# Optimization experiments

Hardware: AMD Instinct MI355X
Metric: run time of the kernel (lower is better)

## Reference

```python
import jax, jax.numpy as jnp
import numpy as np

N = 24000      # total nodes (8000 per node type)
IN_DIM = 128
OUT_DIM = 128
H = 8          # heads
DK = 16        # out_dim // n_heads
T = 3          # node types (hard-coded in edge_attention)
R = 34         # relations (etypes 0..33 per the etype->ntype rules)
EPR = 10000    # edges per relation (DGL applies edge fn per etype)


def _rel_node_types(num_rel):
    # src/dst node type per relation, transcribed from edge_attention
    src_nt = np.array([0 if r <= 9 else (1 if r <= 21 else 2) for r in range(num_rel)], np.int32)
    def _dnt(r):
        if r <= 2 or 10 <= r <= 13 or 22 <= r <= 24:
            return 0
        if 3 <= r <= 6 or 14 <= r <= 17 or 25 <= r <= 28:
            return 1
        return 2
    dst_nt = np.array([_dnt(r) for r in range(num_rel)], np.int32)
    return src_nt, dst_nt

SRC_NT, DST_NT = _rel_node_types(R)


def setup_inputs() -> dict:
    rng = np.random.default_rng(0)
    Nt = N // T  # nodes of type t live in [t*Nt, (t+1)*Nt)
    src = np.stack([rng.integers(SRC_NT[r] * Nt, (SRC_NT[r] + 1) * Nt, EPR) for r in range(R)]).astype(np.int32)
    dst = np.stack([rng.integers(DST_NT[r] * Nt, (DST_NT[r] + 1) * Nt, EPR) for r in range(R)]).astype(np.int32)
    ks = jax.random.split(jax.random.key(0), 10)
    lin = 1.0 / np.sqrt(IN_DIM)
    return {
        'x': jax.random.normal(ks[0], (N, IN_DIM), jnp.float32),
        'src': jnp.asarray(src),
        'dst': jnp.asarray(dst),
        'Wk': jax.random.normal(ks[1], (T, IN_DIM, OUT_DIM), jnp.float32) * lin,
        'bk': jnp.zeros((T, OUT_DIM), jnp.float32),
        'Wq': jax.random.normal(ks[2], (T, IN_DIM, OUT_DIM), jnp.float32) * lin,
        'bq': jnp.zeros((T, OUT_DIM), jnp.float32),
        'Wv': jax.random.normal(ks[3], (T, IN_DIM, OUT_DIM), jnp.float32) * lin,
        'bv': jnp.zeros((T, OUT_DIM), jnp.float32),
        'Wa': jax.random.normal(ks[4], (T, OUT_DIM, OUT_DIM), jnp.float32) * lin,
        'ba': jnp.zeros((T, OUT_DIM), jnp.float32),
        'rel_att': jax.random.normal(ks[5], (R, H, DK, DK), jnp.float32) / np.sqrt(DK),
        'rel_msg': jax.random.normal(ks[6], (R, H, DK, DK), jnp.float32) / np.sqrt(DK),
        'rel_pri': jnp.ones((R, H), jnp.float32),
        'nta': jnp.ones((T,), jnp.float32),
        'nta1': jnp.ones((T,), jnp.float32),
        'skip': jnp.ones((T,), jnp.float32),
        'weight': jnp.ones((1,), jnp.float32),
        'attn_w': jax.random.normal(ks[7], (2 * DK,), jnp.float32) * 0.1,
    }


def reference(x, src, dst, Wk, bk, Wq, bq, Wv, bv, Wa, ba, rel_att, rel_msg, rel_pri, nta, nta1, skip, weight, attn_w):
    ntype = jnp.repeat(jnp.arange(T), N // T)  # node type per node id
    ridx = jnp.arange(N)

    def typed_lin(h, W, b):
        # per-node-type Linear: compute all T projections, select by node type
        return (jnp.einsum('ni,tio->tno', h, W) + b[:, None, :])[ntype, ridx]

    k = typed_lin(x, Wk, bk).reshape(N, H, DK)
    q = typed_lin(x, Wq, bq).reshape(N, H, DK)
    v = typed_lin(x, Wv, bv).reshape(N, H, DK)

    k_src = k[src]                                   # [R, Epr, H, DK]
    q_dst = q[dst]                                   # [R, Epr, H, DK]
    key_t = jnp.einsum('rehd,rhdf->rehf', k_src, rel_att)
    a = (q_dst * key_t).sum(-1) * rel_pri[:, None, :] / np.sqrt(DK)   # [R, Epr, H]
    val = jnp.einsum('rehd,rhdf->rehf', v[src], rel_msg)              # [R, Epr, H, DK]

    # GAT-style concat attention: attn_fc(cat(att_dst*q, att_src*k)) split into two dots
    wq, wk = attn_w[:DK], attn_w[DK:]
    na = jax.nn.leaky_relu(nta1[DST_NT][:, None, None] * (q_dst @ wq)
                           + nta[SRC_NT][:, None, None] * (k_src @ wk))  # [R, Epr, H]

    beta = jax.nn.sigmoid(weight[0])
    s = (a + beta * na).reshape(R * EPR, H)

    # per-(relation, dst-node) segment softmax (DGL mailbox softmax per etype)
    seg = (jnp.arange(R)[:, None] * N + dst).reshape(-1)
    m = jax.ops.segment_max(s, seg, num_segments=R * N)
    e = jnp.exp(s - m[seg])
    den = jax.ops.segment_sum(e, seg, num_segments=R * N)
    att = e / den[seg]

    vf = val.reshape(R * EPR, H, DK)
    h = jax.ops.segment_sum(att[:, :, None] * vf, seg, num_segments=R * N).reshape(R, N, OUT_DIM)

    # cross_reducer='mean': average over relations that delivered messages to a node
    cnt = jax.ops.segment_sum(jnp.ones((R * EPR,), x.dtype), seg, num_segments=R * N).reshape(R, N)
    nrel = jnp.maximum((cnt > 0).astype(x.dtype).sum(0), 1.0)
    t = h.sum(0) / nrel[:, None]                      # [N, OUT_DIM]

    trans = (jnp.einsum('no,top->tnp', t, Wa) + ba[:, None, :])[ntype, ridx]
    alpha = jax.nn.sigmoid(skip)[ntype][:, None]
    return trans * alpha + x * (1.0 - alpha)
```

## Files before the change

kernel.cpp:

```cpp
#include <hip/hip_runtime.h>

#define NN   24000
#define NTP  8000
#define HH   8
#define DKK  16
#define RR   34
#define EPRN 10000
#define NE   (RR*EPRN)
#define NB   (RR*NTP)
#define CAP  16
#define NSCAT ((NE+255)/256)

typedef short short8 __attribute__((ext_vector_type(8)));
typedef float f32x4  __attribute__((ext_vector_type(4)));
typedef _Float16 h2v __attribute__((ext_vector_type(2)));

#if defined(__has_builtin)
# if __has_builtin(__builtin_amdgcn_fdot2)
#  define USE_FDOT2 1
# endif
#endif
#ifndef USE_FDOT2
# define USE_FDOT2 0
#endif

__device__ __forceinline__ int src_nt(int r){ return r<=9?0:(r<=21?1:2); }
__device__ __forceinline__ int dst_nt(int r){
    if (r<=2)  return 0;
    if (r<=6)  return 1;
    if (r<=9)  return 2;
    if (r<=13) return 0;
    if (r<=17) return 1;
    if (r<=21) return 2;
    if (r<=24) return 0;
    if (r<=28) return 1;
    return 2;
}

__device__ __forceinline__ unsigned short bf16rne(float a){
    unsigned int u = __float_as_uint(a);
    u += 0x7fffu + ((u >> 16) & 1u);
    return (unsigned short)(u >> 16);
}
__device__ __forceinline__ unsigned int bf2pack(float a, float b){
    unsigned int ua = __float_as_uint(a);
    unsigned int ub = __float_as_uint(b);
    ua += 0x7fffu + ((ua >> 16) & 1u);
    ub += 0x7fffu + ((ub >> 16) & 1u);
    return (ua >> 16) | (ub & 0xffff0000u);
}
__device__ __forceinline__ unsigned short f16bits(float a){
    _Float16 h = (_Float16)a;
    return __builtin_bit_cast(unsigned short, h);
}

__global__ __launch_bounds__(256) void prep_kernel(
    const float* __restrict__ Wk, const float* __restrict__ Wq,
    const float* __restrict__ Wv, const float* __restrict__ Wa,
    int* __restrict__ counts, unsigned short* __restrict__ wfrag)
{
    const int gid = blockIdx.x * 256 + threadIdx.x;
    if (gid < NB) counts[gid] = 0;
    if (blockIdx.x < 96) {
        const int tile = blockIdx.x * 4 + (threadIdx.x >> 6);
        const int lane = threadIdx.x & 63;
        const float* W;
        int s, n;
        if (tile < 288) {
            s = tile & 3;
            n = (tile >> 2) & 7;
            const int mat = (tile >> 5) % 3;
            const int tau = tile / 96;
            W = (mat == 0 ? Wk : (mat == 1 ? Wq : Wv)) + (size_t)tau * 16384;
        } else {
            const int t2 = tile - 288;
            s = t2 & 3;
            n = (t2 >> 2) & 7;
            const int tau = t2 >> 5;
            W = Wa + (size_t)tau * 16384;
        }
        const int k0  = s * 32 + (lane >> 4) * 8;
        const int col = n * 16 + (lane & 15);
        unsigned short* dstp = wfrag + (size_t)tile * 512 + lane * 8;
        #pragma unroll
        for (int i = 0; i < 8; i++)
            dstp[i] = bf16rne(W[(size_t)(k0 + i) * 128 + col]);
    }
}

__global__ __launch_bounds__(256) void work1(
    const float* __restrict__ x,
    const float* __restrict__ bk, const float* __restrict__ bq,
    const float* __restrict__ bv,
    const unsigned short* __restrict__ wfrag,
    const int* __restrict__ src, const int* __restrict__ dst,
    int* __restrict__ counts, int* __restrict__ esrc16,
    float* __restrict__ qo, unsigned short* __restrict__ kvh)
{
    __shared__ float qs[4][16][132];
    __shared__ unsigned short ksh[4][16][264];

    if (blockIdx.x >= 375) {
        int e = (blockIdx.x - 375) * 256 + threadIdx.x;
        if (e < NE) {
            int r = e / EPRN;
            int b = r * NTP + (dst[e] - dst_nt(r) * NTP);
            int pos = atomicAdd(&counts[b], 1);
            if (pos < CAP) esrc16[(size_t)b * CAP + pos] = src[e];
        }
        return;
    }

    const int rb   = blockIdx.x * 64;
    const int tau  = rb / NTP;
    const int w    = threadIdx.x >> 6;
    const int lane = threadIdx.x & 63;
    const int m    = lane & 15;
    const int quad = lane >> 4;

    short8 af[4];
    {
        const float* xrow = x + (size_t)(rb + w * 16 + m) * 128;
        #pragma unroll
        for (int s = 0; s < 4; s++) {
            float4 f0 = *(const float4*)(xrow + s * 32 + quad * 8);
            float4 f1 = *(const float4*)(xrow + s * 32 + quad * 8 + 4);
            union { unsigned int u[4]; short8 v; } pk;
            pk.u[0] = bf2pack(f0.x, f0.y); pk.u[1] = bf2pack(f0.z, f0.w);
            pk.u[2] = bf2pack(f1.x, f1.y); pk.u[3] = bf2pack(f1.z, f1.w);
            af[s] = pk.v;
        }
    }

    #pragma unroll
    for (int mat = 0; mat < 3; mat++) {
        const float* bias = (mat == 0 ? bk : (mat == 1 ? bq : bv)) + tau * 128;
        #pragma unroll
        for (int n = 0; n < 8; n++) {
            float bb = bias[n * 16 + m];
            f32x4 acc = {bb, bb, bb, bb};
            #pragma unroll
            for (int s = 0; s < 4; s++) {
                const int tile = ((tau * 3 + mat) * 8 + n) * 4 + s;
                short8 bf = *(const short8*)(wfrag + (size_t)tile * 512 + lane * 8);
                acc = __builtin_amdgcn_mfma_f32_16x16x32_bf16(af[s], bf, acc, 0, 0, 0);
            }
            if (mat == 1) {
                #pragma unroll
                for (int i = 0; i < 4; i++) qs[w][quad * 4 + i][n * 16 + m] = acc[i];
            } else {
                const int off = n * 32 + (mat == 0 ? 0 : 16) + m;
                #pragma unroll
                for (int i = 0; i < 4; i++) ksh[w][quad * 4 + i][off] = f16bits(acc[i]);
            }
        }
        if (mat == 1) {
            __syncthreads();
            #pragma unroll
            for (int j = 0; j < 8; j++) {
                const int id = lane + 64 * j;
                const int row = id >> 5, c4 = id & 31;
                float4 v = *(const float4*)(&qs[w][row][c4 * 4]);
                *(float4*)(qo + (size_t)(rb + w * 16 + row) * 128 + c4 * 4) = v;
            }
        }
    }
    __syncthreads();
    #pragma unroll
    for (int j = 0; j < 8; j++) {
        const int id = lane + 64 * j;
        const int row = id >> 5, c8 = id & 31;
        uint4 u = *(const uint4*)(&ksh[w][row][c8 * 8]);
        *(uint4*)(kvh + (size_t)(rb + w * 16 + row) * 256 + c8 * 8) = u;
    }
}

__global__ __launch_bounds__(256) void edge_fused(
    const float* __restrict__ q, const unsigned short* __restrict__ kvh,
    const int* __restrict__ esrc16, const int* __restrict__ counts,
    const float* __restrict__ rel_att, const float* __restrict__ rel_msg,
    const float* __restrict__ rel_pri,
    const float* __restrict__ nta, const float* __restrict__ nta1,
    const float* __restrict__ weightp, const float* __restrict__ attn_w,
    unsigned short* __restrict__ t_bf)
{
    const int tid  = threadIdx.x;
    const int h    = __builtin_amdgcn_readfirstlane((tid >> 6) + 4 * blockIdx.y);
    const int dn   = blockIdx.x * 64 + (tid & 63);
    const int dtau = __builtin_amdgcn_readfirstlane(dn / NTP);
    const int dl   = dn - dtau * NTP;

    float q16[16];
    {
        const float4* qp = (const float4*)(q + (size_t)dn * 128 + h * 16);
        #pragma unroll
        for (int i = 0; i < 4; i++) ((float4*)q16)[i] = qp[i];
    }
    float qwq = 0.f;
    #pragma unroll
    for (int f = 0; f < 16; f++) qwq += q16[f] * attn_w[f];
#if USE_FDOT2
    h2v aw2h[8];
    #pragma unroll
    for (int i = 0; i < 8; i++) {
        h2v t; t[0] = (_Float16)attn_w[16 + 2*i]; t[1] = (_Float16)attn_w[16 + 2*i + 1];
        aw2h[i] = t;
    }
#else
    float aw2[16];
    #pragma unroll
    for (int f = 0; f < 16; f++) aw2[f] = attn_w[16 + f];
#endif
    const float c1   = nta1[dtau];
    const float beta = 1.f / (1.f + expf(-weightp[0]));

    float th[16] = {};
    int nrel = 0;

    for (int r = 0; r < RR; r++) {
        if (dst_nt(r) != dtau) continue;
        const int b   = r * NTP + dl;
        const int beg = b * CAP;
        int cnt = counts[b];
        cnt = cnt < CAP ? cnt : CAP;
        if (!__any(cnt > 0)) continue;

        const float* Ah = rel_att + (((size_t)r * HH + h) << 8);
        float Aq[16];
        #pragma unroll
        for (int d = 0; d < 16; d++) {
            float s = 0.f;
            #pragma unroll
            for (int f = 0; f < 16; f++) s += Ah[d * 16 + f] * q16[f];
            Aq[d] = s;
        }
#if USE_FDOT2
        h2v Aqh[8];
        #pragma unroll
        for (int i = 0; i < 8; i++) {
            h2v t; t[0] = (_Float16)Aq[2*i]; t[1] = (_Float16)Aq[2*i + 1];
            Aqh[i] = t;
        }
#endif

        const float pri = rel_pri[r * HH + h] * 0.25f;
        const float c0  = nta[src_nt(r)];

        int4 e0 = *(const int4*)(esrc16 + beg);
        int4 e1 = *(const int4*)(esrc16 + beg + 4);
        int4 e2 = make_int4(0,0,0,0), e3 = make_int4(0,0,0,0);
        if (__any(cnt > 8)) {
            e2 = *(const int4*)(esrc16 + beg + 8);
            e3 = *(const int4*)(esrc16 + beg + 12);
        }

        float den = 0.f;
        float macc[16] = {};
        #pragma unroll
        for (int ch = 0; ch < 4; ch++) {
            if (!__any(ch * 4 < cnt)) break;
            const int4 cc = (ch == 0) ? e0 : (ch == 1) ? e1 : (ch == 2) ? e2 : e3;
            #pragma unroll
            for (int t = 0; t < 4; t++) {
                const int j = ch * 4 + t;
                if (j < cnt) {
                    const int sn = (t == 0) ? cc.x : (t == 1) ? cc.y : (t == 2) ? cc.z : cc.w;
                    const uint4* kp = (const uint4*)(kvh + (size_t)sn * 256 + h * 32);
                    uint4 u0 = kp[0], u1 = kp[1], u2 = kp[2], u3 = kp[3];
                    float a = 0.f, kwk = 0.f;
#if USE_FDOT2
                    {
                        const unsigned int kw[8] = {u0.x,u0.y,u0.z,u0.w,u1.x,u1.y,u1.z,u1.w};
                        #pragma unroll
                        for (int i = 0; i < 8; i++) {
                            h2v kk2 = __builtin_bit_cast(h2v, kw[i]);
                            a   = __builtin_amdgcn_fdot2(kk2, Aqh[i],  a,   false);
                            kwk = __builtin_amdgcn_fdot2(kk2, aw2h[i], kwk, false);
                        }
                    }
#else
                    {
                        const unsigned int kw[8] = {u0.x,u0.y,u0.z,u0.w,u1.x,u1.y,u1.z,u1.w};
                        #pragma unroll
                        for (int i = 0; i < 8; i++) {
                            h2v kk2 = __builtin_bit_cast(h2v, kw[i]);
                            float k0f = (float)kk2[0], k1f = (float)kk2[1];
                            a   += k0f * Aq[2*i]  + k1f * Aq[2*i + 1];
                            kwk += k0f * aw2[2*i] + k1f * aw2[2*i + 1];
                        }
                    }
#endif
                    float vv[16];
                    {
                        const unsigned int vw[8] = {u2.x,u2.y,u2.z,u2.w,u3.x,u3.y,u3.z,u3.w};
                        #pragma unroll
                        for (int i = 0; i < 8; i++) {
                            h2v v2 = __builtin_bit_cast(h2v, vw[i]);
                            vv[2*i] = (float)v2[0]; vv[2*i + 1] = (float)v2[1];
                        }
                    }
                    float nax = c1 * qwq + c0 * kwk;
                    float na  = nax >= 0.f ? nax : 0.01f * nax;
                    float es  = expf(a * pri + beta * na);
                    den += es;
                    #pragma unroll
                    for (int f = 0; f < 16; f++) macc[f] += es * vv[f];
                }
            }
        }

        if (cnt > 0) {
            nrel++;
            const float inv = 1.f / den;
            const float* Mh = rel_msg + (((size_t)r * HH + h) << 8);
            #pragma unroll
            for (int d = 0; d < 16; d++) {
                float md = macc[d] * inv;
                #pragma unroll
                for (int f = 0; f < 16; f++) th[f] += md * Mh[d * 16 + f];
            }
        }
    }

    const float innv = 1.f / (float)(nrel > 1 ? nrel : 1);
    unsigned short* op = t_bf + (size_t)dn * 128 + h * 16;
    uint4 u0, u1;
    u0.x = bf2pack(th[0] * innv,  th[1] * innv);
    u0.y = bf2pack(th[2] * innv,  th[3] * innv);
    u0.z = bf2pack(th[4] * innv,  th[5] * innv);
    u0.w = bf2pack(th[6] * innv,  th[7] * innv);
    u1.x = bf2pack(th[8] * innv,  th[9] * innv);
    u1.y = bf2pack(th[10] * innv, th[11] * innv);
    u1.z = bf2pack(th[12] * innv, th[13] * innv);
    u1.w = bf2pack(th[14] * innv, th[15] * innv);
    *(uint4*)(op)     = u0;
    *(uint4*)(op + 8) = u1;
}

__global__ __launch_bounds__(256) void final_mfma(
    const unsigned short* __restrict__ t_bf,
    const unsigned short* __restrict__ wfrag,
    const float* __restrict__ ba, const float* __restrict__ skip,
    const float* __restrict__ x, float* __restrict__ out)
{
    __shared__ float os[4][16][132];
    const int rb   = blockIdx.x * 64;
    const int tau  = rb / NTP;
    const int w    = threadIdx.x >> 6;
    const int lane = threadIdx.x & 63;
    const int m    = lane & 15;
    const int quad = lane >> 4;

    short8 af[4];
    {
        const unsigned short* trow = t_bf + (size_t)(rb + w * 16 + m) * 128;
        #pragma unroll
        for (int s = 0; s < 4; s++)
            af[s] = *(const short8*)(trow + s * 32 + quad * 8);
    }

    #pragma unroll
    for (int n = 0; n < 8; n++) {
        float bb = ba[tau * 128 + n * 16 + m];
        f32x4 acc = {bb, bb, bb, bb};
        #pragma unroll
        for (int s = 0; s < 4; s++) {
            const int tile = 288 + tau * 32 + n * 4 + s;
            short8 bf = *(const short8*)(wfrag + (size_t)tile * 512 + lane * 8);
            acc = __builtin_amdgcn_mfma_f32_16x16x32_bf16(af[s], bf, acc, 0, 0, 0);
        }
        #pragma unroll
        for (int i = 0; i < 4; i++) os[w][quad * 4 + i][n * 16 + m] = acc[i];
    }
    __syncthreads();
    const float alpha = 1.f / (1.f + expf(-skip[tau]));
    const float oma   = 1.f - alpha;
    #pragma unroll
    for (int j = 0; j < 8; j++) {
        const int id = lane + 64 * j;
        const int row = id >> 5, c4 = id & 31;
        float4 t  = *(const float4*)(&os[w][row][c4 * 4]);
        const size_t base = (size_t)(rb + w * 16 + row) * 128 + c4 * 4;
        float4 xv = *(const float4*)(x + base);
        float4 o;
        o.x = t.x * alpha + xv.x * oma;
        o.y = t.y * alpha + xv.y * oma;
        o.z = t.z * alpha + xv.z * oma;
        o.w = t.w * alpha + xv.w * oma;
        *(float4*)(out + base) = o;
    }
}

extern "C" void kernel_launch(void* const* d_in, const int* in_sizes, int n_in,
                              void* d_out, int out_size, void* d_ws, size_t ws_size,
                              hipStream_t stream) {
    const float* x       = (const float*)d_in[0];
    const int*   src     = (const int*)  d_in[1];
    const int*   dst     = (const int*)  d_in[2];
    const float* Wk      = (const float*)d_in[3];
    const float* bk      = (const float*)d_in[4];
    const float* Wq      = (const float*)d_in[5];
    const float* bq      = (const float*)d_in[6];
    const float* Wv      = (const float*)d_in[7];
    const float* bv      = (const float*)d_in[8];
    const float* Wa      = (const float*)d_in[9];
    const float* ba      = (const float*)d_in[10];
    const float* rel_att = (const float*)d_in[11];
    const float* rel_msg = (const float*)d_in[12];
    const float* rel_pri = (const float*)d_in[13];
    const float* nta     = (const float*)d_in[14];
    const float* nta1    = (const float*)d_in[15];
    const float* skip    = (const float*)d_in[16];
    const float* weight  = (const float*)d_in[17];
    const float* attn_w  = (const float*)d_in[18];
    float* out = (float*)d_out;

    float* ws    = (float*)d_ws;
    float* q     = ws;
    unsigned short* kvh = (unsigned short*)(q + (size_t)NN * 128);
    unsigned short* t_bf = kvh + (size_t)NN * 256;
    int* counts  = (int*)(t_bf + (size_t)NN * 128);
    int* esrc16  = counts + NB;
    unsigned short* wfrag = (unsigned short*)(esrc16 + (size_t)NB * CAP);

    prep_kernel<<<1063, 256, 0, stream>>>(Wk, Wq, Wv, Wa, counts, wfrag);
    work1<<<375 + NSCAT, 256, 0, stream>>>(x, bk, bq, bv, wfrag,
                                           src, dst, counts, esrc16, q, kvh);
    edge_fused<<<dim3(NN / 64, 2), 256, 0, stream>>>(
        q, kvh, esrc16, counts, rel_att, rel_msg, rel_pri,
        nta, nta1, weight, attn_w, t_bf);
    final_mfma<<<NN / 64, 256, 0, stream>>>(t_bf, wfrag, ba, skip, x, out);
}
```

Measured before the change: 216.1 us.

## Use MFMA for per-relation attention and message transforms, precompute q/k attn dots

The per-lane 16x16 relation attention (Aq) and message matvecs in the edge kernel are replaced with fp16 MFMA tiles. Operands are prepacked in the prep kernel, and message transforms are paired across two relations so each MFMA uses its full K=32. The q·attn_w and k·attn_w dot products move into the projection kernel and are stored per node/head, which removes a per-edge fdot2 chain. Exp is rewritten as exp2 with folded constants. This adds LDS round-trips, fp16 rounding of Aq and messages, and extra workspace buffers.

```diff
diff --git a/kernel.cpp b/kernel.cpp
--- a/kernel.cpp
+++ b/kernel.cpp
@@ -10,8 +10,11 @@
 #define NB   (RR*NTP)
 #define CAP  16
 #define NSCAT ((NE+255)/256)
+#define NPAIR 17
+#define LOG2E 1.4426950408889634f
 
 typedef short short8 __attribute__((ext_vector_type(8)));
+typedef _Float16 half8 __attribute__((ext_vector_type(8)));
 typedef float f32x4  __attribute__((ext_vector_type(4)));
 typedef _Float16 h2v __attribute__((ext_vector_type(2)));
 
@@ -37,6 +40,13 @@
     return 2;
 }
 
+__device__ const int PAIRS[NPAIR][2] = {
+    {0,1},{2,10},{11,12},{13,22},{23,24},
+    {3,4},{5,6},{14,15},{16,17},{25,26},{27,28},
+    {7,8},{9,18},{19,20},{21,29},{30,31},{32,33}};
+__device__ const int PBASE[3] = {0,5,11};
+__device__ const int PCNT[3]  = {5,6,6};
+
 __device__ __forceinline__ unsigned short bf16rne(float a){
     unsigned int u = __float_as_uint(a);
     u += 0x7fffu + ((u >> 16) & 1u);
@@ -57,13 +67,17 @@
 __global__ __launch_bounds__(256) void prep_kernel(
     const float* __restrict__ Wk, const float* __restrict__ Wq,
     const float* __restrict__ Wv, const float* __restrict__ Wa,
-    int* __restrict__ counts, unsigned short* __restrict__ wfrag)
+    const float* __restrict__ rel_att, const float* __restrict__ rel_msg,
+    int* __restrict__ counts, unsigned short* __restrict__ wfrag,
+    unsigned short* __restrict__ fragAtt, unsigned short* __restrict__ fragMsgP)
 {
     const int gid = blockIdx.x * 256 + threadIdx.x;
     if (gid < NB) counts[gid] = 0;
+    const int wv   = threadIdx.x >> 6;
+    const int lane = threadIdx.x & 63;
+    const int m16  = lane & 15, quad = lane >> 4;
     if (blockIdx.x < 96) {
-        const int tile = blockIdx.x * 4 + (threadIdx.x >> 6);
-        const int lane = threadIdx.x & 63;
+        const int tile = blockIdx.x * 4 + wv;
         const float* W;
         int s, n;
         if (tile < 288) {
@@ -79,12 +93,33 @@
             const int tau = t2 >> 5;
             W = Wa + (size_t)tau * 16384;
         }
-        const int k0  = s * 32 + (lane >> 4) * 8;
-        const int col = n * 16 + (lane & 15);
+        const int k0  = s * 32 + quad * 8;
+        const int col = n * 16 + m16;
         unsigned short* dstp = wfrag + (size_t)tile * 512 + lane * 8;
         #pragma unroll
         for (int i = 0; i < 8; i++)
             dstp[i] = bf16rne(W[(size_t)(k0 + i) * 128 + col]);
+    } else if (blockIdx.x < 164) {
+        const int rh = (blockIdx.x - 96) * 4 + wv;
+        half8 v;
+        #pragma unroll
+        for (int i = 0; i < 8; i++) v[i] = (_Float16)0.f;
+        if (quad < 2) {
+            const float* p = rel_att + ((size_t)rh << 8) + m16 * 16 + quad * 8;
+            #pragma unroll
+            for (int i = 0; i < 8; i++) v[i] = (_Float16)p[i];
+        }
+        *(half8*)(fragAtt + ((size_t)rh << 9) + lane * 8) = v;
+    } else if (blockIdx.x < 198) {
+        const int ph = (blockIdx.x - 164) * 4 + wv;
+        const int pair = ph >> 3, hh = ph & 7;
+        const int r  = (quad < 2) ? PAIRS[pair][0] : PAIRS[pair][1];
+        const int kk = (quad & 1) * 8;
+        const float* Mp = rel_msg + (((size_t)r * HH + hh) << 8);
+        half8 v;
+        #pragma unroll
+        for (int i = 0; i < 8; i++) v[i] = (_Float16)Mp[(kk + i) * 16 + m16];
+        *(half8*)(fragMsgP + ((size_t)ph << 9) + lane * 8) = v;
     }
 }
 
@@ -95,7 +130,9 @@
     const unsigned short* __restrict__ wfrag,
     const int* __restrict__ src, const int* __restrict__ dst,
     int* __restrict__ counts, int* __restrict__ esrc16,
-    float* __restrict__ qo, unsigned short* __restrict__ kvh)
+    float* __restrict__ qo, unsigned short* __restrict__ kvh,
+    const float* __restrict__ attn_w,
+    float* __restrict__ qwqA, float* __restrict__ kwkA)
 {
     __shared__ float qs[4][16][132];
     __shared__ unsigned short ksh[4][16][264];
@@ -173,168 +210,204 @@
         uint4 u = *(const uint4*)(&ksh[w][row][c8 * 8]);
         *(uint4*)(kvh + (size_t)(rb + w * 16 + row) * 256 + c8 * 8) = u;
     }
+    #pragma unroll
+    for (int rep = 0; rep < 2; rep++) {
+        const int idx = threadIdx.x + rep * 256;
+        const int row = idx >> 3, hh = idx & 7;
+        const float* qrow = &qs[row >> 4][row & 15][hh * 16];
+        const unsigned short* krow = &ksh[row >> 4][row & 15][hh * 32];
+        float sq = 0.f, sk = 0.f;
+        #pragma unroll
+        for (int f = 0; f < 16; f++) {
+            sq += qrow[f] * attn_w[f];
+            sk += (float)__builtin_bit_cast(_Float16, krow[f]) * attn_w[16 + f];
+        }
+        qwqA[(size_t)(rb + row) * 8 + hh] = sq;
+        kwkA[(size_t)(rb + row) * 8 + hh] = sk;
+    }
 }
 
 __global__ __launch_bounds__(256) void edge_fused(
     const float* __restrict__ q, const unsigned short* __restrict__ kvh,
     const int* __restrict__ esrc16, const int* __restrict__ counts,
-    const float* __restrict__ rel_att, const float* __restrict__ rel_msg,
+    const unsigned short* __restrict__ fragAtt,
+    const unsigned short* __restrict__ fragMsgP,
     const float* __restrict__ rel_pri,
     const float* __restrict__ nta, const float* __restrict__ nta1,
-    const float* __restrict__ weightp, const float* __restrict__ attn_w,
+    const float* __restrict__ weightp,
+    const float* __restrict__ qwqA, const float* __restrict__ kwkA,
     unsigned short* __restrict__ t_bf)
 {
+    __shared__ float tl[4][64][18];
+    __shared__ float md2[4][64][35];
+
     const int tid  = threadIdx.x;
+    const int w    = tid >> 6;
+    const int lane = tid & 63;
     const int h    = __builtin_amdgcn_readfirstlane((tid >> 6) + 4 * blockIdx.y);
-    const int dn   = blockIdx.x * 64 + (tid & 63);
+    const int base = blockIdx.x * 64;
+    const int dn   = base + lane;
     const int dtau = __builtin_amdgcn_readfirstlane(dn / NTP);
     const int dl   = dn - dtau * NTP;
-
-    float q16[16];
-    {
-        const float4* qp = (const float4*)(q + (size_t)dn * 128 + h * 16);
-        #pragma unroll
-        for (int i = 0; i < 4; i++) ((float4*)q16)[i] = qp[i];
-    }
-    float qwq = 0.f;
-    #pragma unroll
-    for (int f = 0; f < 16; f++) qwq += q16[f] * attn_w[f];
+    const int m16  = lane & 15, quad = lane >> 4;
+
+    half8 qf[4];
+    #pragma unroll
+    for (int g = 0; g < 4; g++) {
+        half8 t;
+        #pragma unroll
+        for (int i = 0; i < 8; i++) t[i] = (_Float16)0.f;
+        if (quad < 2) {
+            const float* qp = q + (size_t)(base + g * 16 + m16) * 128 + h * 16 + quad * 8;
+            #pragma unroll
+            for (int i = 0; i < 8; i++) t[i] = (_Float16)qp[i];
+        }
+        qf[g] = t;
+    }
+
+    const float beta = 1.f / (1.f + expf(-weightp[0]));
+    const float bl2e = beta * LOG2E;
+    const float Pq   = bl2e * nta1[dtau] * qwqA[(size_t)dn * 8 + h];
+
+    f32x4 thacc[4];
+    #pragma unroll
+    for (int g = 0; g < 4; g++) { f32x4 z = {0.f,0.f,0.f,0.f}; thacc[g] = z; }
+    int nrel = 0;
+
+    const int pb = PBASE[dtau], pc = PCNT[dtau];
+    for (int p = 0; p < pc; p++) {
+        const int pg = pb + p;
+        int anyPair = 0;
+        #pragma unroll
+        for (int sub = 0; sub < 2; sub++) {
+            const int r = PAIRS[pg][sub];
+            const int b = r * NTP + dl;
+            int cnt = counts[b];
+            cnt = cnt < CAP ? cnt : CAP;
+            float macc[16] = {};
+            float den = 0.f;
+            if (__any(cnt > 0)) {
+                anyPair = 1;
+                half8 Ba = *(const half8*)(fragAtt + (((size_t)r * HH + h) << 9) + lane * 8);
+                #pragma unroll
+                for (int g = 0; g < 4; g++) {
+                    f32x4 aq = {0.f, 0.f, 0.f, 0.f};
+                    aq = __builtin_amdgcn_mfma_f32_16x16x32_f16(qf[g], Ba, aq, 0, 0, 0);
+                    #pragma unroll
+                    for (int i = 0; i < 4; i++)
+                        tl[w][g * 16 + quad * 4 + i][m16] = aq[i];
+                }
 #if USE_FDOT2
-    h2v aw2h[8];
-    #pragma unroll
-    for (int i = 0; i < 8; i++) {
-        h2v t; t[0] = (_Float16)attn_w[16 + 2*i]; t[1] = (_Float16)attn_w[16 + 2*i + 1];
-        aw2h[i] = t;
-    }
+                h2v Aqh[8];
+                #pragma unroll
+                for (int j = 0; j < 8; j++)
+                    Aqh[j] = __builtin_bit_cast(h2v,
+                        __builtin_amdgcn_cvt_pkrtz(tl[w][lane][2*j], tl[w][lane][2*j+1]));
 #else
-    float aw2[16];
-    #pragma unroll
-    for (int f = 0; f < 16; f++) aw2[f] = attn_w[16 + f];
+                float Aqf[16];
+                #pragma unroll
+                for (int d = 0; d < 16; d++) Aqf[d] = tl[w][lane][d];
 #endif
-    const float c1   = nta1[dtau];
-    const float beta = 1.f / (1.f + expf(-weightp[0]));
-
-    float th[16] = {};
-    int nrel = 0;
-
-    for (int r = 0; r < RR; r++) {
-        if (dst_nt(r) != dtau) continue;
-        const int b   = r * NTP + dl;
-        const int beg = b * CAP;
-        int cnt = counts[b];
-        cnt = cnt < CAP ? cnt : CAP;
-        if (!__any(cnt > 0)) continue;
-
-        const float* Ah = rel_att + (((size_t)r * HH + h) << 8);
-        float Aq[16];
-        #pragma unroll
-        for (int d = 0; d < 16; d++) {
-            float s = 0.f;
-            #pragma unroll
-            for (int f = 0; f < 16; f++) s += Ah[d * 16 + f] * q16[f];
-            Aq[d] = s;
-        }
+                const float pri2 = rel_pri[r * HH + h] * (0.25f * LOG2E);
+                const float S    = bl2e * nta[src_nt(r)];
+                const int beg = b * CAP;
+                int4 e0 = *(const int4*)(esrc16 + beg);
+                int4 e1 = *(const int4*)(esrc16 + beg + 4);
+                int4 e2 = make_int4(0,0,0,0), e3 = make_int4(0,0,0,0);
+                if (__any(cnt > 8)) {
+                    e2 = *(const int4*)(esrc16 + beg + 8);
+                    e3 = *(const int4*)(esrc16 + beg + 12);
+                }
+                #pragma unroll
+                for (int ch = 0; ch < 4; ch++) {
+                    if (!__any(ch * 4 < cnt)) break;
+                    const int4 cc = (ch == 0) ? e0 : (ch == 1) ? e1 : (ch == 2) ? e2 : e3;
+                    #pragma unroll
+                    for (int t = 0; t < 4; t++) {
+                        const int j = ch * 4 + t;
+                        if (j < cnt) {
+                            const int sn = (t == 0) ? cc.x : (t == 1) ? cc.y : (t == 2) ? cc.z : cc.w;
+                            const uint4* kp = (const uint4*)(kvh + (size_t)sn * 256 + h * 32);
+                            uint4 u0 = kp[0], u1 = kp[1], u2 = kp[2], u3 = kp[3];
+                            const float kwk = kwkA[(size_t)sn * 8 + h];
+                            float a = 0.f;
 #if USE_FDOT2
-        h2v Aqh[8];
-        #pragma unroll
-        for (int i = 0; i < 8; i++) {
-            h2v t; t[0] = (_Float16)Aq[2*i]; t[1] = (_Float16)Aq[2*i + 1];
-            Aqh[i] = t;
-        }
+                            {
+                                const unsigned int kw[8] = {u0.x,u0.y,u0.z,u0.w,u1.x,u1.y,u1.z,u1.w};
+                                #pragma unroll
+                                for (int i = 0; i < 8; i++)
+                                    a = __builtin_amdgcn_fdot2(__builtin_bit_cast(h2v, kw[i]), Aqh[i], a, false);
+                            }
+#else
+                            {
+                                const unsigned int kw[8] = {u0.x,u0.y,u0.z,u0.w,u1.x,u1.y,u1.z,u1.w};
+                                #pragma unroll
+                                for (int i = 0; i < 8; i++) {
+                                    h2v kk2 = __builtin_bit_cast(h2v, kw[i]);
+                                    a += (float)kk2[0] * Aqf[2*i] + (float)kk2[1] * Aqf[2*i + 1];
+                                }
+                            }
 #endif
-
-        const float pri = rel_pri[r * HH + h] * 0.25f;
-        const float c0  = nta[src_nt(r)];
-
-        int4 e0 = *(const int4*)(esrc16 + beg);
-        int4 e1 = *(const int4*)(esrc16 + beg + 4);
-        int4 e2 = make_int4(0,0,0,0), e3 = make_int4(0,0,0,0);
-        if (__any(cnt > 8)) {
-            e2 = *(const int4*)(esrc16 + beg + 8);
-            e3 = *(const int4*)(esrc16 + beg + 12);
-        }
-
-        float den = 0.f;
-        float macc[16] = {};
-        #pragma unroll
-        for (int ch = 0; ch < 4; ch++) {
-            if (!__any(ch * 4 < cnt)) break;
-            const int4 cc = (ch == 0) ? e0 : (ch == 1) ? e1 : (ch == 2) ? e2 : e3;
-            #pragma unroll
-            for (int t = 0; t < 4; t++) {
-                const int j = ch * 4 + t;
-                if (j < cnt) {
-                    const int sn = (t == 0) ? cc.x : (t == 1) ? cc.y : (t == 2) ? cc.z : cc.w;
-                    const uint4* kp = (const uint4*)(kvh + (size_t)sn * 256 + h * 32);
-                    uint4 u0 = kp[0], u1 = kp[1], u2 = kp[2], u3 = kp[3];
-                    float a = 0.f, kwk = 0.f;
-#if USE_FDOT2
-                    {
-                        const unsigned int kw[8] = {u0.x,u0.y,u0.z,u0.w,u1.x,u1.y,u1.z,u1.w};
-                        #pragma unroll
-                        for (int i = 0; i < 8; i++) {
-                            h2v kk2 = __builtin_bit_cast(h2v, kw[i]);
-                            a   = __builtin_amdgcn_fdot2(kk2, Aqh[i],  a,   false);
-                            kwk = __builtin_amdgcn_fdot2(kk2, aw2h[i], kwk, false);
+                            float vv[16];
+                            {
+                                const unsigned int vw[8] = {u2.x,u2.y,u2.z,u2.w,u3.x,u3.y,u3.z,u3.w};
+                                #pragma unroll
+                                for (int i = 0; i < 8; i++) {
+                                    h2v v2 = __builtin_bit_cast(h2v, vw[i]);
+                                    vv[2*i] = (float)v2[0]; vv[2*i + 1] = (float)v2[1];
+                                }
+                            }
+                            const float y  = fmaf(S, kwk, Pq);
+                            const float na = fmaxf(y, 0.01f * y);
+                            const float es = __builtin_amdgcn_exp2f(fmaf(a, pri2, na));
+                            den += es;
+                            #pragma unroll
+                            for (int f = 0; f < 16; f++) macc[f] += es * vv[f];
                         }
                     }
-#else
-                    {
-                        const unsigned int kw[8] = {u0.x,u0.y,u0.z,u0.w,u1.x,u1.y,u1.z,u1.w};
-                        #pragma unroll
-                        for (int i = 0; i < 8; i++) {
-                            h2v kk2 = __builtin_bit_cast(h2v, kw[i]);
-                            float k0f = (float)kk2[0], k1f = (float)kk2[1];
-                            a   += k0f * Aq[2*i]  + k1f * Aq[2*i + 1];
-                            kwk += k0f * aw2[2*i] + k1f * aw2[2*i + 1];
-                        }
-                    }
-#endif
-                    float vv[16];
-                    {
-                        const unsigned int vw[8] = {u2.x,u2.y,u2.z,u2.w,u3.x,u3.y,u3.z,u3.w};
-                        #pragma unroll
-                        for (int i = 0; i < 8; i++) {
-                            h2v v2 = __builtin_bit_cast(h2v, vw[i]);
-                            vv[2*i] = (float)v2[0]; vv[2*i + 1] = (float)v2[1];
-                        }
-                    }
-                    float nax = c1 * qwq + c0 * kwk;
-                    float na  = nax >= 0.f ? nax : 0.01f * nax;
-                    float es  = expf(a * pri + beta * na);
-                    den += es;
-                    #pragma unroll
-                    for (int f = 0; f < 16; f++) macc[f] += es * vv[f];
                 }
             }
-        }
-
-        if (cnt > 0) {
-            nrel++;
-            const float inv = 1.f / den;
-            const float* Mh = rel_msg + (((size_t)r * HH + h) << 8);
+            float inv = 0.f;
+            if (cnt > 0) { inv = 1.0f / den; nrel++; }
             #pragma unroll
-            for (int d = 0; d < 16; d++) {
-                float md = macc[d] * inv;
-                #pragma unroll
-                for (int f = 0; f < 16; f++) th[f] += md * Mh[d * 16 + f];
+            for (int d = 0; d < 16; d++)
+                md2[w][lane][sub * 16 + d] = macc[d] * inv;
+        }
+        if (anyPair) {
+            half8 Bm = *(const half8*)(fragMsgP + (((size_t)pg * HH + h) << 9) + lane * 8);
+            #pragma unroll
+            for (int g = 0; g < 4; g++) {
+                const float* mp = &md2[w][g * 16 + m16][quad * 8];
+                half8 am;
+                #pragma unroll
+                for (int i = 0; i < 8; i++) am[i] = (_Float16)mp[i];
+                thacc[g] = __builtin_amdgcn_mfma_f32_16x16x32_f16(am, Bm, thacc[g], 0, 0, 0);
             }
         }
     }
 
+    #pragma unroll
+    for (int g = 0; g < 4; g++) {
+        #pragma unroll
+        for (int i = 0; i < 4; i++)
+            tl[w][g * 16 + quad * 4 + i][m16] = thacc[g][i];
+    }
     const float innv = 1.f / (float)(nrel > 1 ? nrel : 1);
+    float t16[16];
+    #pragma unroll
+    for (int f = 0; f < 16; f++) t16[f] = tl[w][lane][f] * innv;
     unsigned short* op = t_bf + (size_t)dn * 128 + h * 16;
-    uint4 u0, u1;
-    u0.x = bf2pack(th[0] * innv,  th[1] * innv);
-    u0.y = bf2pack(th[2] * innv,  th[3] * innv);
-    u0.z = bf2pack(th[4] * innv,  th[5] * innv);
-    u0.w = bf2pack(th[6] * innv,  th[7] * innv);
-    u1.x = bf2pack(th[8] * innv,  th[9] * innv);
-    u1.y = bf2pack(th[10] * innv, th[11] * innv);
-    u1.z = bf2pack(th[12] * innv, th[13] * innv);
-    u1.w = bf2pack(th[14] * innv, th[15] * innv);
-    *(uint4*)(op)     = u0;
-    *(uint4*)(op + 8) = u1;
+    uint4 o0, o1;
+    o0.x = bf2pack(t16[0],  t16[1]);
+    o0.y = bf2pack(t16[2],  t16[3]);
+    o0.z = bf2pack(t16[4],  t16[5]);
+    o0.w = bf2pack(t16[6],  t16[7]);
+    o1.x = bf2pack(t16[8],  t16[9]);
+    o1.y = bf2pack(t16[10], t16[11]);
+    o1.z = bf2pack(t16[12], t16[13]);
+    o1.w = bf2pack(t16[14], t16[15]);
+    *(uint4*)(op)     = o0;
+    *(uint4*)(op + 8) = o1;
 }
 
 __global__ __launch_bounds__(256) void final_mfma(
@@ -422,12 +495,18 @@
     int* counts  = (int*)(t_bf + (size_t)NN * 128);
     int* esrc16  = counts + NB;
     unsigned short* wfrag = (unsigned short*)(esrc16 + (size_t)NB * CAP);
-
-    prep_kernel<<<1063, 256, 0, stream>>>(Wk, Wq, Wv, Wa, counts, wfrag);
+    unsigned short* fragAtt  = wfrag + 384 * 512;
+    unsigned short* fragMsgP = fragAtt + 272 * 512;
+    float* qwqA  = (float*)(fragMsgP + 136 * 512);
+    float* kwkA  = qwqA + (size_t)NN * 8;
+
+    prep_kernel<<<1063, 256, 0, stream>>>(Wk, Wq, Wv, Wa, rel_att, rel_msg,
+                                          counts, wfrag, fragAtt, fragMsgP);
     work1<<<375 + NSCAT, 256, 0, stream>>>(x, bk, bq, bv, wfrag,
-                                           src, dst, counts, esrc16, q, kvh);
+                                           src, dst, counts, esrc16, q, kvh,
+                                           attn_w, qwqA, kwkA);
     edge_fused<<<dim3(NN / 64, 2), 256, 0, stream>>>(
-        q, kvh, esrc16, counts, rel_att, rel_msg, rel_pri,
-        nta, nta1, weight, attn_w, t_bf);
+        q, kvh, esrc16, counts, fragAtt, fragMsgP, rel_pri,
+        nta, nta1, weight, qwqA, kwkA, t_bf);
     final_mfma<<<NN / 64, 256, 0, stream>>>(t_bf, wfrag, ba, skip, x, out);
 }
```

Result: no change. 217.1 us (+0.5%).
